# Performance work log

Measured on AMD Instinct MI355X. Metric: run time of the kernel, lower is better.

Reference implementation:

```python
import jax, jax.numpy as jnp
import numpy as np

FS = 100.0  # sampling_rate


def _csd(x, NF):
    # CrossSpectralDensity: per-batch, all-pairs cross-correlation (torch conv1d padding='same'),
    # then rfft over time and mean over the F*F pair axis.
    B, T, F = x.shape
    left = (T - 1) // 2                      # torch 'same' padding: left=floor, right=ceil
    xpad = jnp.pad(x, ((0, 0), (left, T - 1 - left), (0, 0)))

    def per_batch(xp_b, x_b):
        # xp_b: (Tp,F) padded signals, x_b: (T,F) kernels
        lhs = xp_b.T[:, None, :]             # (F_i, 1, Tp)  signals as batch
        rhs = x_b.T[:, None, :]              # (F_j, 1, T)   kernels as out-channels
        # lax conv = cross-correlation (no flip), matching torch conv1d
        return jax.lax.conv_general_dilated(lhs, rhs, (1,), 'VALID')  # (F_i, F_j, T)

    convs = jax.vmap(per_batch)(xpad, x)                    # (B, F, F, T)
    convs = jnp.transpose(convs, (0, 3, 1, 2)).reshape(B, T, F * F)  # pair index i*F+j
    cf = jnp.fft.rfft(convs, axis=1, norm='ortho')[:, :NF, :]
    return cf.mean(axis=-1, keepdims=True)                  # (B, NF, 1)


def reference(x, W_proj, b_proj, W_gate, b_gate, mag_w, mag_b, phase_w, phase_b, ln_gamma, ln_beta):
    B, H, F = x.shape
    NF = mag_w.shape[0]                     # = H//2 + 1 (threshold = fs/2 keeps all freqs)
    hid = W_proj.shape[1]

    fft = jnp.fft.rfft(x, axis=1, norm='ortho')[:, :NF, :]  # (B, NF, F) complex
    fft = fft + _csd(x, NF)

    mag = jnp.abs(fft)
    ang = jnp.angle(fft)
    freqs = jnp.arange(NF, dtype=x.dtype) * (FS / H)        # rfftfreq(H, 1/FS)
    ff = jnp.concatenate([
        jnp.stack([mag, jnp.sin(ang), jnp.cos(ang)], axis=-1),
        jnp.broadcast_to(freqs[None, :, None, None], (B, NF, F, 1)),
    ], axis=-1)                                             # (B, NF, F, 4)

    # per-freq projection layers all share one weight (ModuleList of the same module)
    proj = jax.nn.relu(jnp.einsum('bnfk,kh->bnfh', ff, W_proj) + b_proj)  # (B, NF, F, hid)

    # cat over freq along last dim -> (B, F, NF*hid), element [.., i*hid+h] = proj[:, i, :, h]
    flat = jnp.transpose(proj, (0, 2, 1, 3)).reshape(B, F, NF * hid)
    g = flat @ W_gate + b_gate                              # (B, F, NF)
    g = g * jax.nn.sigmoid(g)                               # SimpleGate (SiLU)
    w = jnp.transpose(jax.nn.sigmoid(g), (0, 2, 1))         # (B, NF, F)

    # Complexifier per frequency (distinct weights per freq); proj is already >=0 (relu idempotent)
    m = jax.nn.relu(jnp.einsum('bnfh,nh->bnf', proj, mag_w) + mag_b[None, :, None])
    ph = 2.0 * jnp.pi * jax.nn.sigmoid(jnp.einsum('bnfh,nh->bnf', proj, phase_w) + phase_b[None, :, None])
    new_fft = m * jnp.cos(ph) + 1j * (m * jnp.sin(ph))      # (B, NF, F) complex

    wf = w * new_fft + (1.0 - w) * fft
    wf = jnp.pad(wf, ((0, 0), (0, H // 2 + 1 - NF), (0, 0)))  # no-op here (NF == H//2+1)
    recon = jnp.fft.irfft(wf, axis=1, norm='ortho')         # (B, H, F)

    # LayerNorm(input_size) over residual
    y = recon + x
    mu = y.mean(axis=-1, keepdims=True)
    var = ((y - mu) ** 2).mean(axis=-1, keepdims=True)
    return (y - mu) / jnp.sqrt(var + 1e-5) * ln_gamma + ln_beta


def setup_inputs():
    key = jax.random.key(0)
    ks = jax.random.split(key, 12)
    B, H, F, HID = 128, 512, 16, 64
    NF = H // 2 + 1  # 257
    s = 0.05
    return {
        'x': jax.random.normal(ks[0], (B, H, F), jnp.float32),
        'W_proj': jax.random.normal(ks[1], (4, HID), jnp.float32) * s,
        'b_proj': jax.random.normal(ks[2], (HID,), jnp.float32) * s,
        'W_gate': jax.random.normal(ks[3], (NF * HID, NF), jnp.float32) * 0.01,
        'b_gate': jax.random.normal(ks[4], (NF,), jnp.float32) * s,
        'mag_w': jax.random.normal(ks[5], (NF, HID), jnp.float32) * s,
        'mag_b': jax.random.normal(ks[6], (NF,), jnp.float32) * s,
        'phase_w': jax.random.normal(ks[7], (NF, HID), jnp.float32) * s,
        'phase_b': jax.random.normal(ks[8], (NF,), jnp.float32) * s,
        'ln_gamma': jnp.ones((F,), jnp.float32),
        'ln_beta': jnp.zeros((F,), jnp.float32),
    }
```

## Files before the change

### kernel.cpp

```cpp
#include <hip/hip_runtime.h>


#define NF_ 257
#define NKB 514
#define FRAGS 263168
#define SPK 16
#define SORTHO 0.04419417382f

typedef __attribute__((ext_vector_type(8))) short short8;
typedef __attribute__((ext_vector_type(4))) float floatx4;

__device__ __forceinline__ unsigned int f2bf(float x) {
  union { float f; unsigned int u; } v; v.f = x;
  return (v.u + 0x7FFFu + ((v.u >> 16) & 1u)) >> 16;
}
__device__ __forceinline__ float bf2f(unsigned int u16) {
  union { unsigned int u; float f; } v; v.u = u16 << 16;
  return v.f;
}

__global__ __launch_bounds__(256) void k_prep(const float* __restrict__ x,
                                              const float* __restrict__ Wg,
                                              float* __restrict__ csd,
                                              unsigned short* __restrict__ Bf,
                                              unsigned short* __restrict__ TWf,
                                              unsigned short* __restrict__ ITWf) {
  __shared__ float sl[768];
  __shared__ float ac[257];
  __shared__ float red[4];
  const int tid = threadIdx.x;
  const int blk = blockIdx.x;

  if (blk < 128) {
    const int bb = blk;
    for (int t = tid; t < 768; t += 256) {
      float v = 0.f;
      if (t < 512) {
        const float4* xp = (const float4*)(x + (bb * 512 + t) * 16);
        float4 a = xp[0], b = xp[1], c = xp[2], d = xp[3];
        v = a.x + a.y + a.z + a.w + b.x + b.y + b.z + b.w +
            c.x + c.y + c.z + c.w + d.x + d.y + d.z + d.w;
      }
      sl[t] = v;
    }
    __syncthreads();
    {
      float a0 = 0.f, a1 = 0.f, a2 = 0.f, a3 = 0.f;
      for (int tau = 0; tau < 512; tau += 4) {
        float4 u = *(const float4*)&sl[tau];
        a0 = fmaf(u.x, sl[tau + tid], a0);
        a1 = fmaf(u.y, sl[tau + tid + 1], a1);
        a2 = fmaf(u.z, sl[tau + tid + 2], a2);
        a3 = fmaf(u.w, sl[tau + tid + 3], a3);
      }
      ac[tid] = (a0 + a1) + (a2 + a3);
    }
    {
      float p = sl[tid] * sl[tid + 256];
#pragma unroll
      for (int off = 32; off; off >>= 1) p += __shfl_down(p, off);
      if ((tid & 63) == 0) red[tid >> 6] = p;
    }
    __syncthreads();
    if (tid == 0) ac[256] = red[0] + red[1] + red[2] + red[3];
    __syncthreads();
    const float S1 = SORTHO / 256.f;
    const int k = tid;
    float sth, cth;
    __sincosf((float)k * 0.01227184630f, &sth, &cth);
    float c = 1.f, s = 0.f, re = 0.f, im = 0.f;
    float re256 = 0.f, sg = 1.f;
    for (int t = 0; t < 512; ++t) {
      int d = t - 255;
      float ov = ac[d < 0 ? -d : d];
      re = fmaf(ov, c, re);
      im = fmaf(-ov, s, im);
      re256 = fmaf(ov, sg, re256);
      sg = -sg;
      float nc = fmaf(c, cth, -s * sth);
      s = fmaf(s, cth, c * sth);
      c = nc;
    }
    *(float2*)(csd + (bb * NF_ + k) * 2) = make_float2(re * S1, im * S1);
    if (tid == 0)
      *(float2*)(csd + (bb * NF_ + 256) * 2) = make_float2(re256 * S1, 0.f);
    return;
  }

  if (blk < 2698) {
    const int slot = (blk - 128) * 256 + tid;
    const int nblk = slot / 32896;
    const int rem = slot - nblk * 32896;
    const int kb = rem >> 6, lane = rem & 63;
    const int n = nblk * 16 + (lane & 15);
    const int k0 = kb * 32 + (lane >> 4) * 8;
    unsigned int w[4];
#pragma unroll
    for (int jp = 0; jp < 4; ++jp) {
      float v0 = (n < NF_) ? Wg[(k0 + jp * 2) * NF_ + n] : 0.f;
      float v1 = (n < NF_) ? Wg[(k0 + jp * 2 + 1) * NF_ + n] : 0.f;
      w[jp] = f2bf(v0) | (f2bf(v1) << 16);
    }
    *(uint4*)(Bf + (size_t)slot * 8) = make_uint4(w[0], w[1], w[2], w[3]);
    return;
  }

  if (blk < 2834) {
    const int slot = (blk - 2698) * 256 + tid;
    const int tile = slot >> 10, rem = slot & 1023;
    const int ks = rem >> 6, quad = (rem >> 4) & 3, l15 = rem & 15;
    const int grow = tile * 16 + l15;
    unsigned int pk[4];
#pragma unroll
    for (int jp = 0; jp < 4; ++jp) {
      float v0 = 0.f, v1 = 0.f;
      if (grow < 514) {
        const int k = grow >> 1;
        const int t0 = ks * 32 + quad * 8 + jp * 2;
        float s0, c0, s1, c1;
        __sincosf((float)((k * t0) & 511) * 0.01227184630f, &s0, &c0);
        __sincosf((float)((k * (t0 + 1)) & 511) * 0.01227184630f, &s1, &c1);
        v0 = (grow & 1) ? -s0 * SORTHO : c0 * SORTHO;
        v1 = (grow & 1) ? -s1 * SORTHO : c1 * SORTHO;
      }
      pk[jp] = f2bf(v0) | (f2bf(v1) << 16);
    }
    *(uint4*)(TWf + slot * 8) = make_uint4(pk[0], pk[1], pk[2], pk[3]);
    return;
  }

  {
    const int slot = (blk - 2834) * 256 + tid;
    const int tile = slot / 1088, rem = slot % 1088;
    const int ks = rem >> 6, sub = rem & 63;
    const int quad = sub >> 4, l15 = sub & 15;
    const int t = tile * 16 + l15;
    unsigned int pk[4];
#pragma unroll
    for (int jp = 0; jp < 4; ++jp) {
      float v0 = 0.f, v1 = 0.f;
#pragma unroll
      for (int h = 0; h < 2; ++h) {
        const int kidx = ks * 32 + quad * 8 + jp * 2 + h;
        float v = 0.f;
        if (kidx < 514) {
          const int k = kidx >> 1;
          const float hw = (k == 0 || k == 256) ? SORTHO : 2.f * SORTHO;
          float s, c;
          __sincosf((float)((k * t) & 511) * 0.01227184630f, &s, &c);
          v = (kidx & 1) ? -s * hw : c * hw;
        }
        if (h == 0) v0 = v; else v1 = v;
      }
      pk[jp] = f2bf(v0) | (f2bf(v1) << 16);
    }
    *(uint4*)(ITWf + slot * 8) = make_uint4(pk[0], pk[1], pk[2], pk[3]);
  }
}

__global__ __launch_bounds__(512) void k_spec(const float* __restrict__ x,
                                              const unsigned short* __restrict__ TWf,
                                              const float* __restrict__ csd,
                                              const float* __restrict__ W_proj,
                                              const float* __restrict__ b_proj,
                                              const float* __restrict__ mag_w,
                                              const float* __restrict__ mag_b,
                                              const float* __restrict__ phase_w,
                                              const float* __restrict__ phase_b,
                                              float* __restrict__ fftc,
                                              float* __restrict__ nf,
                                              unsigned short* __restrict__ Af) {
  __shared__ __align__(16) unsigned short Xs[16 * 512];
  __shared__ float4 wp4[64];
  __shared__ float bps[64];
  const int tid = threadIdx.x, mh = blockIdx.x, bb = blockIdx.y;
  if (tid < 64) {
    wp4[tid] = make_float4(W_proj[tid], W_proj[64 + tid], W_proj[128 + tid],
                           W_proj[192 + tid]);
    bps[tid] = b_proj[tid];
  }
#pragma unroll
  for (int it = 0; it < 16; ++it) {
    int e = it * 512 + tid;
    int f = e & 15, t = e >> 4;
    float val = x[(bb * 512 + t) * 16 + f];
    Xs[f * 512 + (((t >> 3) ^ (f & 7)) * 8) + (t & 7)] = (unsigned short)f2bf(val);
  }
  __syncthreads();
  const int lane = tid & 63, wave = tid >> 6;
  const int l15 = lane & 15, quad = lane >> 4;
  floatx4 acc0 = {0,0,0,0}, acc1 = {0,0,0,0}, acc2 = {0,0,0,0};
  const int g0 = mh * 17 + wave, g1 = g0 + 8, g2 = mh * 17 + 16;
#pragma unroll
  for (int ks = 0; ks < 16; ++ks) {
    short8 bf = *(const short8*)&Xs[l15 * 512 + (((ks * 4 + quad) ^ (l15 & 7)) * 8)];
    short8 af0 = *(const short8*)(TWf + g0 * 8192 + ks * 512 + quad * 128 + l15 * 8);
    short8 af1 = *(const short8*)(TWf + g1 * 8192 + ks * 512 + quad * 128 + l15 * 8);
    acc0 = __builtin_amdgcn_mfma_f32_16x16x32_bf16(af0, bf, acc0, 0, 0, 0);
    acc1 = __builtin_amdgcn_mfma_f32_16x16x32_bf16(af1, bf, acc1, 0, 0, 0);
    if (wave == 0) {
      short8 af2 = *(const short8*)(TWf + g2 * 8192 + ks * 512 + quad * 128 + l15 * 8);
      acc2 = __builtin_amdgcn_mfma_f32_16x16x32_bf16(af2, bf, acc2, 0, 0, 0);
    }
  }
#pragma unroll
  for (int i = 0; i < 3; ++i) {
    if (i == 2 && wave != 0) break;
    const int g = (i == 0) ? g0 : (i == 1) ? g1 : g2;
    floatx4 a = (i == 0) ? acc0 : (i == 1) ? acc1 : acc2;
#pragma unroll
    for (int kp = 0; kp < 2; ++kp) {
      const int grow = g * 16 + quad * 4 + kp * 2;
      if (grow < 514) {
        const int k = grow >> 1;
        float2 cz = *(const float2*)(csd + (bb * NF_ + k) * 2);
        float re = a[kp * 2] + cz.x;
        float im = a[kp * 2 + 1] + cz.y;
        const int ofc = ((bb * NF_ + k) * 16 + l15) * 2;
        *(float2*)(fftc + ofc) = make_float2(re, im);
        float d = re * re + im * im;
        float ir = d > 0.f ? rsqrtf(d) : 0.f;
        float mag = d * ir;
        float sn = im * ir;
        float cs = d > 0.f ? re * ir : 1.f;
        float fr = (float)k * 0.1953125f;
        float am = 0.f, ap = 0.f;
        unsigned short* abase = Af + ((size_t)bb * NKB + k * 2) * 512 + l15 * 8;
        const float4* mwp = (const float4*)(mag_w + k * 64);
        const float4* pwp = (const float4*)(phase_w + k * 64);
#pragma unroll
        for (int hg = 0; hg < 8; ++hg) {
          float4 mw0 = mwp[hg * 2], mw1 = mwp[hg * 2 + 1];
          float4 pw0 = pwp[hg * 2], pw1 = pwp[hg * 2 + 1];
          unsigned int w[4];
#pragma unroll
          for (int j = 0; j < 8; ++j) {
            const int h = hg * 8 + j;
            float4 wv = wp4[h];
            float p = fmaf(mag, wv.x, fmaf(sn, wv.y, fmaf(cs, wv.z,
                      fmaf(fr, wv.w, bps[h]))));
            p = fmaxf(p, 0.f);
            float mwj = (j < 4) ? (&mw0.x)[j] : (&mw1.x)[j - 4];
            float pwj = (j < 4) ? (&pw0.x)[j] : (&pw1.x)[j - 4];
            am = fmaf(p, mwj, am);
            ap = fmaf(p, pwj, ap);
            unsigned int pb16 = f2bf(p);
            if (j & 1) w[j >> 1] |= pb16 << 16; else w[j >> 1] = pb16;
          }
          *(uint4*)(abase + (hg >> 2) * 512 + (hg & 3) * 128) =
              make_uint4(w[0], w[1], w[2], w[3]);
        }
        float m = fmaxf(am + mag_b[k], 0.f);
        float ph = 6.28318530718f / (1.f + __expf(-(ap + phase_b[k])));
        float sp_, cp_;
        __sincosf(ph, &sp_, &cp_);
        *(float2*)(nf + ofc) = make_float2(m * cp_, m * sp_);
      }
    }
  }
}

__global__ __launch_bounds__(256, 2) void k_gemm(const unsigned short* __restrict__ Af,
                                                 const unsigned short* __restrict__ Bf,
                                                 unsigned short* __restrict__ gpart) {
  __shared__ __align__(16) unsigned short As[2][4096];
  const int tid = threadIdx.x;
  const int sp = blockIdx.x, mgg = blockIdx.y;
  const int lane = tid & 63, wv = tid >> 6;
  const int p0 = (NF_ * sp) >> 4, p1 = (NF_ * (sp + 1)) >> 4;
  const int nsteps = p1 - p0;
  const int c0 = wv * 2, c1 = wv * 2 + 1;
  const unsigned short* aSrc0 = Af + (size_t)(mgg * 4 + (c0 & 3)) * FRAGS
                                + (size_t)(p0 * 2 + (c0 >> 2)) * 512 + lane * 8;
  const unsigned short* aSrc1 = Af + (size_t)(mgg * 4 + (c1 & 3)) * FRAGS
                                + (size_t)(p0 * 2 + (c1 >> 2)) * 512 + lane * 8;
  const unsigned short* pb = Bf + (size_t)(wv * 5) * FRAGS
                             + (size_t)(p0 * 2) * 512 + lane * 8;

  floatx4 acc[4][5];
#pragma unroll
  for (int mi = 0; mi < 4; ++mi)
#pragma unroll
    for (int nn = 0; nn < 5; ++nn) acc[mi][nn] = (floatx4){0.f, 0.f, 0.f, 0.f};

  uint4 ra0 = *(const uint4*)aSrc0;
  uint4 ra1 = *(const uint4*)aSrc1;
  short8 bX[5], bY[5];
#pragma unroll
  for (int nn = 0; nn < 5; ++nn) {
    bX[nn] = *(const short8*)(pb + (size_t)nn * FRAGS);
    bY[nn] = *(const short8*)(pb + (size_t)nn * FRAGS + 512);
  }

  for (int s = 0; s < nsteps; ++s) {
    unsigned short* dst = &As[s & 1][0];
    *(uint4*)(dst + c0 * 512 + lane * 8) = ra0;
    *(uint4*)(dst + c1 * 512 + lane * 8) = ra1;
    if (s + 1 < nsteps) {
      aSrc0 += 1024; aSrc1 += 1024;
      ra0 = *(const uint4*)aSrc0;
      ra1 = *(const uint4*)aSrc1;
    }
    __builtin_amdgcn_sched_barrier(0);
    asm volatile("s_waitcnt lgkmcnt(0)" ::: "memory");
    __builtin_amdgcn_s_barrier();
    __builtin_amdgcn_sched_barrier(0);
    const unsigned short* rb = &As[s & 1][0];
    {
      short8 a0 = *(const short8*)(rb + 0 * 512 + lane * 8);
      short8 a1 = *(const short8*)(rb + 1 * 512 + lane * 8);
      short8 a2 = *(const short8*)(rb + 2 * 512 + lane * 8);
      short8 a3 = *(const short8*)(rb + 3 * 512 + lane * 8);
#pragma unroll
      for (int nn = 0; nn < 5; ++nn) {
        acc[0][nn] = __builtin_amdgcn_mfma_f32_16x16x32_bf16(a0, bX[nn], acc[0][nn], 0, 0, 0);
        acc[1][nn] = __builtin_amdgcn_mfma_f32_16x16x32_bf16(a1, bX[nn], acc[1][nn], 0, 0, 0);
        acc[2][nn] = __builtin_amdgcn_mfma_f32_16x16x32_bf16(a2, bX[nn], acc[2][nn], 0, 0, 0);
        acc[3][nn] = __builtin_amdgcn_mfma_f32_16x16x32_bf16(a3, bX[nn], acc[3][nn], 0, 0, 0);
      }
      if (s + 1 < nsteps) {
#pragma unroll
        for (int nn = 0; nn < 5; ++nn)
          bX[nn] = *(const short8*)(pb + (size_t)nn * FRAGS + 1024);
      }
    }
    {
      short8 a0 = *(const short8*)(rb + 4 * 512 + lane * 8);
      short8 a1 = *(const short8*)(rb + 5 * 512 + lane * 8);
      short8 a2 = *(const short8*)(rb + 6 * 512 + lane * 8);
      short8 a3 = *(const short8*)(rb + 7 * 512 + lane * 8);
#pragma unroll
      for (int nn = 0; nn < 5; ++nn) {
        acc[0][nn] = __builtin_amdgcn_mfma_f32_16x16x32_bf16(a0, bY[nn], acc[0][nn], 0, 0, 0);
        acc[1][nn] = __builtin_amdgcn_mfma_f32_16x16x32_bf16(a1, bY[nn], acc[1][nn], 0, 0, 0);
        acc[2][nn] = __builtin_amdgcn_mfma_f32_16x16x32_bf16(a2, bY[nn], acc[2][nn], 0, 0, 0);
        acc[3][nn] = __builtin_amdgcn_mfma_f32_16x16x32_bf16(a3, bY[nn], acc[3][nn], 0, 0, 0);
      }
      if (s + 1 < nsteps) {
#pragma unroll
        for (int nn = 0; nn < 5; ++nn)
          bY[nn] = *(const short8*)(pb + (size_t)nn * FRAGS + 1536);
        pb += 1024;
      }
    }
  }

#pragma unroll
  for (int mi = 0; mi < 4; ++mi)
#pragma unroll
    for (int nn = 0; nn < 5; ++nn) {
      unsigned int lo = f2bf(acc[mi][nn][0]) | (f2bf(acc[mi][nn][1]) << 16);
      unsigned int hi = f2bf(acc[mi][nn][2]) | (f2bf(acc[mi][nn][3]) << 16);
      *(uint2*)(gpart + ((((size_t)sp * 128 + mgg * 4 + mi) * 20) + wv * 5 + nn) * 256
                + lane * 4) = make_uint2(lo, hi);
    }
}

__global__ __launch_bounds__(512) void k_recong(const float* __restrict__ fftc,
                                                const float* __restrict__ nfb,
                                                const unsigned short* __restrict__ gpart,
                                                const float* __restrict__ b_gate,
                                                const unsigned short* __restrict__ ITWf,
                                                const float* __restrict__ x,
                                                const float* __restrict__ ln_g,
                                                const float* __restrict__ ln_b,
                                                float* __restrict__ out) {
  __shared__ __align__(16) unsigned short WFs[16 * 576];
  __shared__ float wls[16 * 257];
  const int tid = threadIdx.x, th = blockIdx.x, bb = blockIdx.y;
  const unsigned short* gpb = gpart + (size_t)bb * 5120;
  for (int t = tid; t < 1088; t += 512) {
    const int n = ((t >> 6) << 4) + (t & 15);
    if (n < NF_) {
      const int quad = (t >> 4) & 3;
      const float bg = b_gate[n];
      float g0 = bg, g1 = bg, g2 = bg, g3 = bg;
#pragma unroll
      for (int s2 = 0; s2 < SPK; ++s2) {
        uint2 v = *(const uint2*)(gpb + (size_t)s2 * 655360 + (size_t)t * 4);
        g0 += bf2f(v.x & 0xFFFFu); g1 += bf2f(v.x >> 16);
        g2 += bf2f(v.y & 0xFFFFu); g3 += bf2f(v.y >> 16);
      }
      float gv[4] = {g0, g1, g2, g3};
#pragma unroll
      for (int r = 0; r < 4; ++r) {
        float g = gv[r];
        float sg = 1.f / (1.f + __expf(-g));
        float gs = g * sg;
        wls[(quad * 4 + r) * 257 + n] = 1.f / (1.f + __expf(-gs));
      }
    }
  }
  __syncthreads();
#pragma unroll
  for (int it = 0; it < 17; ++it) {
    int e = it * 512 + tid;
    int f = e & 15, row = e >> 4;
    float val = 0.f;
    if (row < 514) {
      int k = row >> 1, ri = row & 1;
      int base = ((bb * NF_ + k) * 16 + f) * 2 + ri;
      float fz = fftc[base], nz = nfb[base];
      float wv = wls[f * 257 + k];
      val = fz + wv * (nz - fz);
    }
    WFs[f * 576 + (((row >> 3) ^ (f & 7)) * 8) + (row & 7)] = (unsigned short)f2bf(val);
  }
  __syncthreads();
  const int lane = tid & 63, wave = tid >> 6;
  const int l15 = lane & 15, quad = lane >> 4;
  const float gg = ln_g[l15], gb = ln_b[l15];
  floatx4 acc[2];
  acc[0] = (floatx4){0.f, 0.f, 0.f, 0.f};
  acc[1] = (floatx4){0.f, 0.f, 0.f, 0.f};
  const int tg0 = th * 16 + wave, tg1 = tg0 + 8;
#pragma unroll
  for (int ks = 0; ks < 17; ++ks) {
    short8 bf = *(const short8*)&WFs[l15 * 576 + (((ks * 4 + quad) ^ (l15 & 7)) * 8)];
    short8 af0 = *(const short8*)(ITWf + tg0 * 8704 + ks * 512 + quad * 128 + l15 * 8);
    short8 af1 = *(const short8*)(ITWf + tg1 * 8704 + ks * 512 + quad * 128 + l15 * 8);
    acc[0] = __builtin_amdgcn_mfma_f32_16x16x32_bf16(af0, bf, acc[0], 0, 0, 0);
    acc[1] = __builtin_amdgcn_mfma_f32_16x16x32_bf16(af1, bf, acc[1], 0, 0, 0);
  }
#pragma unroll
  for (int i = 0; i < 2; ++i) {
    const int tg = (i == 0) ? tg0 : tg1;
#pragma unroll
    for (int r = 0; r < 4; ++r) {
      const int t = tg * 16 + quad * 4 + r;
      float y = acc[i][r] + x[(bb * 512 + t) * 16 + l15];
      float s1 = y, s2 = y * y;
#pragma unroll
      for (int m = 1; m < 16; m <<= 1) {
        s1 += __shfl_xor(s1, m);
        s2 += __shfl_xor(s2, m);
      }
      float mu = s1 * 0.0625f;
      float var = s2 * 0.0625f - mu * mu;
      float rs = rsqrtf(var + 1e-5f);
      out[(bb * 512 + t) * 16 + l15] = (y - mu) * rs * gg + gb;
    }
  }
}

extern "C" void kernel_launch(void* const* d_in, const int* in_sizes, int n_in,
                              void* d_out, int out_size, void* d_ws, size_t ws_size,
                              hipStream_t stream) {
  const float* x = (const float*)d_in[0];
  const float* W_proj = (const float*)d_in[1];
  const float* b_proj = (const float*)d_in[2];
  const float* W_gate = (const float*)d_in[3];
  const float* b_gate = (const float*)d_in[4];
  const float* mag_w = (const float*)d_in[5];
  const float* mag_b = (const float*)d_in[6];
  const float* phase_w = (const float*)d_in[7];
  const float* phase_b = (const float*)d_in[8];
  const float* ln_g = (const float*)d_in[9];
  const float* ln_b = (const float*)d_in[10];
  float* out = (float*)d_out;
  float* ws = (float*)d_ws;

  float* fftc = ws;
  float* nfb = ws + 1052672;
  float* csd = ws + 2631680;
  unsigned short* Afrag = (unsigned short*)(ws + 2697472);
  unsigned short* Bfrag = (unsigned short*)(ws + 19540224);
  unsigned short* gpart = (unsigned short*)(ws + 22171904);
  unsigned short* TWf = (unsigned short*)(ws + 27414784);
  unsigned short* ITWf = (unsigned short*)(ws + 27554048);

  hipLaunchKernelGGL(k_prep, dim3(2970), dim3(256), 0, stream,
                     x, W_gate, csd, Bfrag, TWf, ITWf);
  hipLaunchKernelGGL(k_spec, dim3(2, 128), dim3(512), 0, stream, x, TWf, csd,
                     W_proj, b_proj, mag_w, mag_b, phase_w, phase_b,
                     fftc, nfb, Afrag);
  hipLaunchKernelGGL(k_gemm, dim3(16, 32), dim3(256), 0, stream, Afrag, Bfrag, gpart);
  hipLaunchKernelGGL(k_recong, dim3(2, 128), dim3(512), 0, stream, fftc, nfb, gpart,
                     b_gate, ITWf, x, ln_g, ln_b, out);
}
```

Baseline: 180.9 us.

## Retile split-K GEMM into 2x2 warp tiles loading A directly to registers

After: 194.9 us. 1.08x slower.

```diff
diff --git a/kernel.cpp b/kernel.cpp
--- a/kernel.cpp
+++ b/kernel.cpp
@@ -260,22 +260,20 @@
   }
 }
 
-__global__ __launch_bounds__(256, 2) void k_gemm(const unsigned short* __restrict__ Af,
-                                                 const unsigned short* __restrict__ Bf,
-                                                 unsigned short* __restrict__ gpart) {
-  __shared__ __align__(16) unsigned short As[2][4096];
+__global__ __launch_bounds__(256) void k_gemm(const unsigned short* __restrict__ Af,
+                                              const unsigned short* __restrict__ Bf,
+                                              unsigned short* __restrict__ gpart) {
   const int tid = threadIdx.x;
-  const int sp = blockIdx.x, mgg = blockIdx.y;
+  const int mn = blockIdx.x, sp = blockIdx.y;
+  const int mb = mn >> 1, nb = mn & 1;
   const int lane = tid & 63, wv = tid >> 6;
-  const int p0 = (NF_ * sp) >> 4, p1 = (NF_ * (sp + 1)) >> 4;
-  const int nsteps = p1 - p0;
-  const int c0 = wv * 2, c1 = wv * 2 + 1;
-  const unsigned short* aSrc0 = Af + (size_t)(mgg * 4 + (c0 & 3)) * FRAGS
-                                + (size_t)(p0 * 2 + (c0 >> 2)) * 512 + lane * 8;
-  const unsigned short* aSrc1 = Af + (size_t)(mgg * 4 + (c1 & 3)) * FRAGS
-                                + (size_t)(p0 * 2 + (c1 >> 2)) * 512 + lane * 8;
-  const unsigned short* pb = Bf + (size_t)(wv * 5) * FRAGS
-                             + (size_t)(p0 * 2) * 512 + lane * 8;
+  const int wm = wv & 1, wn = wv >> 1;
+  const int i0 = (NF_ * sp) >> 4, i1 = (NF_ * (sp + 1)) >> 4;
+  const int nk = (i1 - i0) * 2;
+  const unsigned short* pa = Af + (size_t)(mb * 8 + wm * 4) * FRAGS
+                             + (size_t)(i0 * 2) * 512 + lane * 8;
+  const unsigned short* pb = Bf + (size_t)(nb * 10 + wn * 5) * FRAGS
+                             + (size_t)(i0 * 2) * 512 + lane * 8;
 
   floatx4 acc[4][5];
 #pragma unroll
@@ -283,75 +281,63 @@
 #pragma unroll
     for (int nn = 0; nn < 5; ++nn) acc[mi][nn] = (floatx4){0.f, 0.f, 0.f, 0.f};
 
-  uint4 ra0 = *(const uint4*)aSrc0;
-  uint4 ra1 = *(const uint4*)aSrc1;
-  short8 bX[5], bY[5];
+  short8 aX[4], aY[4], bX[5], bY[5];
+#pragma unroll
+  for (int mi = 0; mi < 4; ++mi) {
+    aX[mi] = *(const short8*)(pa + (size_t)mi * FRAGS);
+    aY[mi] = *(const short8*)(pa + (size_t)mi * FRAGS + 512);
+  }
 #pragma unroll
   for (int nn = 0; nn < 5; ++nn) {
     bX[nn] = *(const short8*)(pb + (size_t)nn * FRAGS);
     bY[nn] = *(const short8*)(pb + (size_t)nn * FRAGS + 512);
   }
-
+  const int nsteps = (nk - 2) >> 1;
   for (int s = 0; s < nsteps; ++s) {
-    unsigned short* dst = &As[s & 1][0];
-    *(uint4*)(dst + c0 * 512 + lane * 8) = ra0;
-    *(uint4*)(dst + c1 * 512 + lane * 8) = ra1;
-    if (s + 1 < nsteps) {
-      aSrc0 += 1024; aSrc1 += 1024;
-      ra0 = *(const uint4*)aSrc0;
-      ra1 = *(const uint4*)aSrc1;
-    }
-    __builtin_amdgcn_sched_barrier(0);
-    asm volatile("s_waitcnt lgkmcnt(0)" ::: "memory");
-    __builtin_amdgcn_s_barrier();
-    __builtin_amdgcn_sched_barrier(0);
-    const unsigned short* rb = &As[s & 1][0];
-    {
-      short8 a0 = *(const short8*)(rb + 0 * 512 + lane * 8);
-      short8 a1 = *(const short8*)(rb + 1 * 512 + lane * 8);
-      short8 a2 = *(const short8*)(rb + 2 * 512 + lane * 8);
-      short8 a3 = *(const short8*)(rb + 3 * 512 + lane * 8);
-#pragma unroll
-      for (int nn = 0; nn < 5; ++nn) {
-        acc[0][nn] = __builtin_amdgcn_mfma_f32_16x16x32_bf16(a0, bX[nn], acc[0][nn], 0, 0, 0);
-        acc[1][nn] = __builtin_amdgcn_mfma_f32_16x16x32_bf16(a1, bX[nn], acc[1][nn], 0, 0, 0);
-        acc[2][nn] = __builtin_amdgcn_mfma_f32_16x16x32_bf16(a2, bX[nn], acc[2][nn], 0, 0, 0);
-        acc[3][nn] = __builtin_amdgcn_mfma_f32_16x16x32_bf16(a3, bX[nn], acc[3][nn], 0, 0, 0);
-      }
-      if (s + 1 < nsteps) {
-#pragma unroll
-        for (int nn = 0; nn < 5; ++nn)
-          bX[nn] = *(const short8*)(pb + (size_t)nn * FRAGS + 1024);
-      }
-    }
-    {
-      short8 a0 = *(const short8*)(rb + 4 * 512 + lane * 8);
-      short8 a1 = *(const short8*)(rb + 5 * 512 + lane * 8);
-      short8 a2 = *(const short8*)(rb + 6 * 512 + lane * 8);
-      short8 a3 = *(const short8*)(rb + 7 * 512 + lane * 8);
-#pragma unroll
-      for (int nn = 0; nn < 5; ++nn) {
-        acc[0][nn] = __builtin_amdgcn_mfma_f32_16x16x32_bf16(a0, bY[nn], acc[0][nn], 0, 0, 0);
-        acc[1][nn] = __builtin_amdgcn_mfma_f32_16x16x32_bf16(a1, bY[nn], acc[1][nn], 0, 0, 0);
-        acc[2][nn] = __builtin_amdgcn_mfma_f32_16x16x32_bf16(a2, bY[nn], acc[2][nn], 0, 0, 0);
-        acc[3][nn] = __builtin_amdgcn_mfma_f32_16x16x32_bf16(a3, bY[nn], acc[3][nn], 0, 0, 0);
-      }
-      if (s + 1 < nsteps) {
-#pragma unroll
-        for (int nn = 0; nn < 5; ++nn)
-          bY[nn] = *(const short8*)(pb + (size_t)nn * FRAGS + 1536);
-        pb += 1024;
-      }
-    }
-  }
-
+#pragma unroll
+    for (int mi = 0; mi < 4; ++mi)
+#pragma unroll
+      for (int nn = 0; nn < 5; ++nn)
+        acc[mi][nn] = __builtin_amdgcn_mfma_f32_16x16x32_bf16(aX[mi], bX[nn],
+                                                              acc[mi][nn], 0, 0, 0);
+#pragma unroll
+    for (int mi = 0; mi < 4; ++mi) aX[mi] = *(const short8*)(pa + (size_t)mi * FRAGS + 1024);
+#pragma unroll
+    for (int nn = 0; nn < 5; ++nn) bX[nn] = *(const short8*)(pb + (size_t)nn * FRAGS + 1024);
+#pragma unroll
+    for (int mi = 0; mi < 4; ++mi)
+#pragma unroll
+      for (int nn = 0; nn < 5; ++nn)
+        acc[mi][nn] = __builtin_amdgcn_mfma_f32_16x16x32_bf16(aY[mi], bY[nn],
+                                                              acc[mi][nn], 0, 0, 0);
+#pragma unroll
+    for (int mi = 0; mi < 4; ++mi) aY[mi] = *(const short8*)(pa + (size_t)mi * FRAGS + 1536);
+#pragma unroll
+    for (int nn = 0; nn < 5; ++nn) bY[nn] = *(const short8*)(pb + (size_t)nn * FRAGS + 1536);
+    pa += 1024; pb += 1024;
+  }
 #pragma unroll
   for (int mi = 0; mi < 4; ++mi)
 #pragma unroll
+    for (int nn = 0; nn < 5; ++nn)
+      acc[mi][nn] = __builtin_amdgcn_mfma_f32_16x16x32_bf16(aX[mi], bX[nn],
+                                                            acc[mi][nn], 0, 0, 0);
+#pragma unroll
+  for (int mi = 0; mi < 4; ++mi)
+#pragma unroll
+    for (int nn = 0; nn < 5; ++nn)
+      acc[mi][nn] = __builtin_amdgcn_mfma_f32_16x16x32_bf16(aY[mi], bY[nn],
+                                                            acc[mi][nn], 0, 0, 0);
+
+#pragma unroll
+  for (int mi = 0; mi < 4; ++mi)
+#pragma unroll
     for (int nn = 0; nn < 5; ++nn) {
+      const int mfrag = mb * 8 + wm * 4 + mi;
+      const int nblk = nb * 10 + wn * 5 + nn;
       unsigned int lo = f2bf(acc[mi][nn][0]) | (f2bf(acc[mi][nn][1]) << 16);
       unsigned int hi = f2bf(acc[mi][nn][2]) | (f2bf(acc[mi][nn][3]) << 16);
-      *(uint2*)(gpart + ((((size_t)sp * 128 + mgg * 4 + mi) * 20) + wv * 5 + nn) * 256
+      *(uint2*)(gpart + (((size_t)sp * 128 + mfrag) * 20 + nblk) * 256
                 + lane * 4) = make_uint2(lo, hi);
     }
 }
@@ -474,7 +460,7 @@
   hipLaunchKernelGGL(k_spec, dim3(2, 128), dim3(512), 0, stream, x, TWf, csd,
                      W_proj, b_proj, mag_w, mag_b, phase_w, phase_b,
                      fftc, nfb, Afrag);
-  hipLaunchKernelGGL(k_gemm, dim3(16, 32), dim3(256), 0, stream, Afrag, Bfrag, gpart);
+  hipLaunchKernelGGL(k_gemm, dim3(32, 16), dim3(256), 0, stream, Afrag, Bfrag, gpart);
   hipLaunchKernelGGL(k_recong, dim3(2, 128), dim3(512), 0, stream, fftc, nfb, gpart,
                      b_gate, ITWf, x, ln_g, ln_b, out);
 }
```

## Split spectrum kernel into FFT GEMM and separate per-element projection kernel

Applied to the files above, without the earlier changes.

Result: no change. 183.5 us (+1.4%).

```diff
diff --git a/kernel.cpp b/kernel.cpp
--- a/kernel.cpp
+++ b/kernel.cpp
@@ -158,27 +158,12 @@
   }
 }
 
-__global__ __launch_bounds__(512) void k_spec(const float* __restrict__ x,
+__global__ __launch_bounds__(512) void k_fftg(const float* __restrict__ x,
                                               const unsigned short* __restrict__ TWf,
                                               const float* __restrict__ csd,
-                                              const float* __restrict__ W_proj,
-                                              const float* __restrict__ b_proj,
-                                              const float* __restrict__ mag_w,
-                                              const float* __restrict__ mag_b,
-                                              const float* __restrict__ phase_w,
-                                              const float* __restrict__ phase_b,
-                                              float* __restrict__ fftc,
-                                              float* __restrict__ nf,
-                                              unsigned short* __restrict__ Af) {
+                                              float* __restrict__ fftc) {
   __shared__ __align__(16) unsigned short Xs[16 * 512];
-  __shared__ float4 wp4[64];
-  __shared__ float bps[64];
   const int tid = threadIdx.x, mh = blockIdx.x, bb = blockIdx.y;
-  if (tid < 64) {
-    wp4[tid] = make_float4(W_proj[tid], W_proj[64 + tid], W_proj[128 + tid],
-                           W_proj[192 + tid]);
-    bps[tid] = b_proj[tid];
-  }
 #pragma unroll
   for (int it = 0; it < 16; ++it) {
     int e = it * 512 + tid;
@@ -209,55 +194,65 @@
     const int g = (i == 0) ? g0 : (i == 1) ? g1 : g2;
     floatx4 a = (i == 0) ? acc0 : (i == 1) ? acc1 : acc2;
 #pragma unroll
-    for (int kp = 0; kp < 2; ++kp) {
-      const int grow = g * 16 + quad * 4 + kp * 2;
+    for (int r = 0; r < 4; ++r) {
+      const int grow = g * 16 + quad * 4 + r;
       if (grow < 514) {
-        const int k = grow >> 1;
-        float2 cz = *(const float2*)(csd + (bb * NF_ + k) * 2);
-        float re = a[kp * 2] + cz.x;
-        float im = a[kp * 2 + 1] + cz.y;
-        const int ofc = ((bb * NF_ + k) * 16 + l15) * 2;
-        *(float2*)(fftc + ofc) = make_float2(re, im);
-        float d = re * re + im * im;
-        float ir = d > 0.f ? rsqrtf(d) : 0.f;
-        float mag = d * ir;
-        float sn = im * ir;
-        float cs = d > 0.f ? re * ir : 1.f;
-        float fr = (float)k * 0.1953125f;
-        float am = 0.f, ap = 0.f;
-        unsigned short* abase = Af + ((size_t)bb * NKB + k * 2) * 512 + l15 * 8;
-        const float4* mwp = (const float4*)(mag_w + k * 64);
-        const float4* pwp = (const float4*)(phase_w + k * 64);
-#pragma unroll
-        for (int hg = 0; hg < 8; ++hg) {
-          float4 mw0 = mwp[hg * 2], mw1 = mwp[hg * 2 + 1];
-          float4 pw0 = pwp[hg * 2], pw1 = pwp[hg * 2 + 1];
-          unsigned int w[4];
-#pragma unroll
-          for (int j = 0; j < 8; ++j) {
-            const int h = hg * 8 + j;
-            float4 wv = wp4[h];
-            float p = fmaf(mag, wv.x, fmaf(sn, wv.y, fmaf(cs, wv.z,
-                      fmaf(fr, wv.w, bps[h]))));
-            p = fmaxf(p, 0.f);
-            float mwj = (j < 4) ? (&mw0.x)[j] : (&mw1.x)[j - 4];
-            float pwj = (j < 4) ? (&pw0.x)[j] : (&pw1.x)[j - 4];
-            am = fmaf(p, mwj, am);
-            ap = fmaf(p, pwj, ap);
-            unsigned int pb16 = f2bf(p);
-            if (j & 1) w[j >> 1] |= pb16 << 16; else w[j >> 1] = pb16;
-          }
-          *(uint4*)(abase + (hg >> 2) * 512 + (hg & 3) * 128) =
-              make_uint4(w[0], w[1], w[2], w[3]);
-        }
-        float m = fmaxf(am + mag_b[k], 0.f);
-        float ph = 6.28318530718f / (1.f + __expf(-(ap + phase_b[k])));
-        float sp_, cp_;
-        __sincosf(ph, &sp_, &cp_);
-        *(float2*)(nf + ofc) = make_float2(m * cp_, m * sp_);
-      }
-    }
-  }
+        const int k = grow >> 1, ri = grow & 1;
+        fftc[((bb * NF_ + k) * 16 + l15) * 2 + ri] =
+            a[r] + csd[(bb * NF_ + k) * 2 + ri];
+      }
+    }
+  }
+}
+
+__global__ __launch_bounds__(256) void k_new(const float* __restrict__ fftc,
+                                             const float* __restrict__ W_proj,
+                                             const float* __restrict__ b_proj,
+                                             const float* __restrict__ mag_w,
+                                             const float* __restrict__ mag_b,
+                                             const float* __restrict__ phase_w,
+                                             const float* __restrict__ phase_b,
+                                             float* __restrict__ nf,
+                                             unsigned short* __restrict__ Af) {
+  __shared__ float wp[256], bp[64];
+  const int tid = threadIdx.x;
+  wp[tid] = W_proj[tid];
+  if (tid < 64) bp[tid] = b_proj[tid];
+  __syncthreads();
+  const int idx = blockIdx.x * 256 + tid;
+  const int bn = idx >> 4, f = idx & 15;
+  const int n = bn % NF_, b = bn / NF_;
+  float2 z = *(const float2*)(fftc + idx * 2);
+  float d = z.x * z.x + z.y * z.y;
+  float ir = d > 0.f ? rsqrtf(d) : 0.f;
+  float mag = d * ir;
+  float sn = z.y * ir;
+  float cs = d > 0.f ? z.x * ir : 1.f;
+  float fr = (float)n * 0.1953125f;
+  float am = 0.f, ap = 0.f;
+  unsigned short* abase = Af + ((size_t)b * NKB + n * 2) * 512 + f * 8;
+#pragma unroll
+  for (int hg = 0; hg < 8; ++hg) {
+    unsigned int w[4];
+#pragma unroll
+    for (int j = 0; j < 8; ++j) {
+      const int h = hg * 8 + j;
+      float p = fmaf(mag, wp[h], fmaf(sn, wp[64 + h], fmaf(cs, wp[128 + h],
+                fmaf(fr, wp[192 + h], bp[h]))));
+      p = fmaxf(p, 0.f);
+      am = fmaf(p, mag_w[n * 64 + h], am);
+      ap = fmaf(p, phase_w[n * 64 + h], ap);
+      unsigned int pb16 = f2bf(p);
+      if (j & 1) w[j >> 1] |= pb16 << 16; else w[j >> 1] = pb16;
+    }
+    *(uint4*)(abase + (hg >> 2) * 512 + (hg & 3) * 128) =
+        make_uint4(w[0], w[1], w[2], w[3]);
+  }
+  float m = fmaxf(am + mag_b[n], 0.f);
+  float ph = 6.28318530718f / (1.f + __expf(-(ap + phase_b[n])));
+  float sp, cp;
+  __sincosf(ph, &sp, &cp);
+  *(float2*)(nf + idx * 2) = make_float2(m * cp, m * sp);
 }
 
 __global__ __launch_bounds__(256, 2) void k_gemm(const unsigned short* __restrict__ Af,
@@ -471,9 +466,9 @@
 
   hipLaunchKernelGGL(k_prep, dim3(2970), dim3(256), 0, stream,
                      x, W_gate, csd, Bfrag, TWf, ITWf);
-  hipLaunchKernelGGL(k_spec, dim3(2, 128), dim3(512), 0, stream, x, TWf, csd,
-                     W_proj, b_proj, mag_w, mag_b, phase_w, phase_b,
-                     fftc, nfb, Afrag);
+  hipLaunchKernelGGL(k_fftg, dim3(2, 128), dim3(512), 0, stream, x, TWf, csd, fftc);
+  hipLaunchKernelGGL(k_new, dim3(2056), dim3(256), 0, stream, fftc, W_proj, b_proj,
+                     mag_w, mag_b, phase_w, phase_b, nfb, Afrag);
   hipLaunchKernelGGL(k_gemm, dim3(16, 32), dim3(256), 0, stream, Afrag, Bfrag, gpart);
   hipLaunchKernelGGL(k_recong, dim3(2, 128), dim3(512), 0, stream, fftc, nfb, gpart,
                      b_gate, ITWf, x, ln_g, ln_b, out);
```
